# Kernel tuning notes

Measured on AMD Instinct MI355X. Metric: run time of the kernel, lower is better.

Reference implementation:

```python
import jax, jax.numpy as jnp
import numpy as np

N, D = 4096, 1024
DH = D // 2  # head=2 (forced by the two-way chunk unpack in the source)
W_SCALE = 0.02


def setup_inputs() -> dict:
    key = jax.random.key(0)
    ks = jax.random.split(key, 7)
    mk = lambda k: jax.random.normal(k, (DH, DH), dtype=jnp.float32) * W_SCALE
    return {
        "x": jax.random.normal(ks[0], (N, D), dtype=jnp.float32),
        "Wq1": mk(ks[1]), "Wq2": mk(ks[2]),
        "Wk1": mk(ks[3]), "Wk2": mk(ks[4]),
        "Wv1": mk(ks[5]), "Wv2": mk(ks[6]),
    }


def _head(xh, Wq, Wk, Wv):
    # xh: (Dh, N) channel-major chunk, W*: (Dh, Dh) 1x1-conv weights
    q = Wq @ xh  # (Dh, N)
    k = Wk @ xh  # (Dh, N)
    v = Wv @ xh  # (Dh, N)
    # QK_T conv: Sc[i, j] = k_i . q_j ; permuted -> S[j, i] = q_j . k_i
    S = jnp.einsum("dn,dm->nm", q, k)  # (N, N), no softmax / no 1/sqrt(Dh) in source
    # Sc_V conv with S as weight: out[j, d] = sum_i S[j, i] * v[d, i]
    return jnp.einsum("nm,dm->nd", S, v)  # (N, Dh)


def reference(x, Wq1, Wq2, Wk1, Wk2, Wv1, Wv2):
    xT = x.T  # (D, N), matches x.permute(1,0).reshape(D, N, 1)
    x1, x2 = xT[:DH], xT[DH:]
    o1 = _head(x1, Wq1, Wk1, Wv1)
    o2 = _head(x2, Wq2, Wk2, Wv2)
    return jnp.concatenate([o1, o2], axis=1)  # (N, D), matches concat+squeeze
```

## Files before the change

### kernel.cpp

```cpp
#include <hip/hip_runtime.h>
#include <hip/hip_bf16.h>

#define N_ROWS 4096
#define D_FULL 1024
#define DHALF  512
#define GSPLIT 8

typedef __attribute__((ext_vector_type(8))) short bf16x8;
typedef __attribute__((ext_vector_type(8))) unsigned short u16x8;
typedef __attribute__((ext_vector_type(4))) float f32x4;

__device__ __forceinline__ unsigned short f2b(float f) {
  __hip_bfloat16 h = __float2bfloat16(f);
  union { __hip_bfloat16 b; unsigned short u; } cv;
  cv.b = h;
  return cv.u;
}
__device__ __forceinline__ float b2f(unsigned short u) {
  union { unsigned int i; float f; } cv;
  cv.i = ((unsigned int)u) << 16;
  return cv.f;
}

__device__ __forceinline__ void load_lds16(const void* g, void* l) {
  __builtin_amdgcn_global_load_lds(
      (const __attribute__((address_space(1))) unsigned int*)g,
      (__attribute__((address_space(3))) unsigned int*)l, 16, 0, 0);
}

template<int N> __device__ __forceinline__ void vmwait() {
  if constexpr (N == 0)       asm volatile("s_waitcnt vmcnt(0)" ::: "memory");
  else if constexpr (N == 2)  asm volatile("s_waitcnt vmcnt(2)" ::: "memory");
  else if constexpr (N == 3)  asm volatile("s_waitcnt vmcnt(3)" ::: "memory");
  else if constexpr (N == 4)  asm volatile("s_waitcnt vmcnt(4)" ::: "memory");
  else if constexpr (N == 6)  asm volatile("s_waitcnt vmcnt(6)" ::: "memory");
  else if constexpr (N == 8)  asm volatile("s_waitcnt vmcnt(8)" ::: "memory");
  else                        asm volatile("s_waitcnt vmcnt(16)" ::: "memory");
}
__device__ __forceinline__ void barx() {
  __builtin_amdgcn_sched_barrier(0);
  __builtin_amdgcn_s_barrier();
  __builtin_amdgcn_sched_barrier(0);
}
__device__ __forceinline__ int b4inc(int b) { return (b + 1) & 3; }

__device__ __forceinline__ void cvt_tile(const float* __restrict__ src, int lds_,
                                         unsigned short* __restrict__ dst, int ldd,
                                         unsigned short* __restrict__ dstT, int ldt,
                                         int n0, int c0) {
  __shared__ unsigned short tile[64][66];
  const int t  = threadIdx.x;
  const int r  = t >> 2;
  const int cq = (t & 3) * 16;

  unsigned short loc[16];
  #pragma unroll
  for (int i = 0; i < 4; ++i) {
    float4 v = *reinterpret_cast<const float4*>(&src[(size_t)(n0 + r) * lds_ + c0 + cq + i * 4]);
    loc[i*4+0] = f2b(v.x); loc[i*4+1] = f2b(v.y); loc[i*4+2] = f2b(v.z); loc[i*4+3] = f2b(v.w);
  }
  if (dst) {
    u16x8 a, b;
    #pragma unroll
    for (int i = 0; i < 8; ++i) { a[i] = loc[i]; b[i] = loc[8+i]; }
    unsigned short* p = &dst[(size_t)(n0 + r) * ldd + c0 + cq];
    *reinterpret_cast<u16x8*>(p)     = a;
    *reinterpret_cast<u16x8*>(p + 8) = b;
  }
  if (dstT) {
    #pragma unroll
    for (int i = 0; i < 8; ++i) {
      ushort2 w2; w2.x = loc[2*i]; w2.y = loc[2*i+1];
      *reinterpret_cast<ushort2*>(&tile[r][cq + 2*i]) = w2;
    }
    __syncthreads();
    const int c  = t >> 2;
    const int ng = (t & 3) * 16;
    unsigned short o[16];
    #pragma unroll
    for (int i = 0; i < 16; ++i) o[i] = tile[ng + i][c];
    u16x8 a, b;
    #pragma unroll
    for (int i = 0; i < 8; ++i) { a[i] = o[i]; b[i] = o[8+i]; }
    unsigned short* p = &dstT[(size_t)(c0 + c) * ldt + n0 + ng];
    *reinterpret_cast<u16x8*>(p)     = a;
    *reinterpret_cast<u16x8*>(p + 8) = b;
  }
}

__global__ __launch_bounds__(256) void k_cvt_all(const float* __restrict__ x,
                                                 const float* __restrict__ w0, const float* __restrict__ w1,
                                                 const float* __restrict__ w2, const float* __restrict__ w3,
                                                 const float* __restrict__ w4, const float* __restrict__ w5,
                                                 unsigned short* __restrict__ xb,
                                                 unsigned short* __restrict__ xT,
                                                 unsigned short* __restrict__ Wb,
                                                 unsigned short* __restrict__ WbT) {
  const int b = blockIdx.x;
  if (b < 1024) {
    cvt_tile(x, D_FULL, xb, D_FULL, xT, N_ROWS, (b >> 4) * 64, (b & 15) * 64);
  } else {
    const int b2 = b - 1024;
    const int z = b2 >> 6, t = b2 & 63;
    const float* w;
    switch (z) {
      case 0: w = w0; break; case 1: w = w1; break; case 2: w = w2; break;
      case 3: w = w3; break; case 4: w = w4; break; default: w = w5; break;
    }
    const size_t HH = (size_t)DHALF * DHALF;
    unsigned short* d  = (z >= 4) ? (Wb  + z * HH) : nullptr;
    unsigned short* dT = (z <  4) ? (WbT + z * HH) : nullptr;
    cvt_tile(w, DHALF, d, DHALF, dT, DHALF, (t >> 3) * 64, (t & 7) * 64);
  }
}

__global__ __launch_bounds__(256) void k_gp(const unsigned short* __restrict__ xT,
                                            const unsigned short* __restrict__ WbT,
                                            unsigned short* __restrict__ Gp,
                                            unsigned short* __restrict__ P) {
  const int o = blockIdx.x;
  const int c = o & 7, j = o >> 3;

  const unsigned short* Ab;
  const unsigned short* Bb;
  unsigned short* Cb;
  int lda, m0, n0;
  bool sameAB = false;
  const long long HH = 262144;
  if (j < 4) {
    const int pp = c * 4 + j;
    const int h = pp >> 4, tile = pp & 15;
    Ab = WbT + (size_t)h * HH;
    Bb = WbT + (size_t)(2 + h) * HH;
    Cb = P + (size_t)h * HH;
    lda = DHALF;
    m0 = (tile >> 2) * 128; n0 = (tile & 3) * 128;
  } else {
    const int g = c * 20 + (j - 4);
    const int slice = g / 10, p = g - slice * 10;
    const int h = slice >> 3, s = slice & 7;
    const int ti = (p < 4) ? 0 : (p < 7) ? 1 : (p < 9) ? 2 : 3;
    const int tj = (p < 4) ? p : (p < 7) ? p - 3 : (p < 9) ? p - 5 : 3;
    Ab = xT + (size_t)h * DHALF * N_ROWS + s * (N_ROWS / GSPLIT);
    Bb = Ab;
    Cb = Gp + (size_t)slice * HH;
    lda = N_ROWS;
    m0 = ti * 128; n0 = tj * 128;
    sameAB = (ti == tj);
  }

  __shared__ __align__(16) unsigned short lds[4][2][128 * 32];

  const int tid  = threadIdx.x;
  const int lane = tid & 63;
  const int wave = tid >> 6;
  const int wm = (wave >> 1) * 64;
  const int wn = (wave & 1) * 64;
  const int fr = lane & 15;
  const int kg = (lane >> 4) * 8;

  const int srow = wave * 32 + (lane >> 2);
  const int scol = (lane & 3) * 8;
  const unsigned short* gA0 = Ab + (size_t)(m0 + srow) * lda + scol;
  const unsigned short* gA1 = gA0 + (size_t)16 * lda;
  const unsigned short* gB0 = Bb + (size_t)(n0 + srow) * lda + scol;
  const unsigned short* gB1 = gB0 + (size_t)16 * lda;
  const int stOff = wave * 1024;

  f32x4 acc[4][4] = {};

  auto STAGE = [&](int buf, int t) {
    const int kofs = t * 32;
    load_lds16(gA0 + kofs, &lds[buf][0][stOff]);
    load_lds16(gA1 + kofs, &lds[buf][0][stOff + 512]);
    if (!sameAB) {
      load_lds16(gB0 + kofs, &lds[buf][1][stOff]);
      load_lds16(gB1 + kofs, &lds[buf][1][stOff + 512]);
    }
  };
  auto COMPUTE = [&](int buf) {
    const unsigned short* la = &lds[buf][0][0];
    const unsigned short* lb = sameAB ? la : &lds[buf][1][0];
    bf16x8 af[4], bf[4];
    #pragma unroll
    for (int f = 0; f < 4; ++f) {
      af[f] = *reinterpret_cast<const bf16x8*>(&la[(wm + f * 16 + fr) * 32 + kg]);
      bf[f] = *reinterpret_cast<const bf16x8*>(&lb[(wn + f * 16 + fr) * 32 + kg]);
    }
    #pragma unroll
    for (int fm = 0; fm < 4; ++fm)
      #pragma unroll
      for (int fn = 0; fn < 4; ++fn)
        acc[fm][fn] = __builtin_amdgcn_mfma_f32_16x16x32_bf16(af[fm], bf[fn], acc[fm][fn], 0, 0, 0);
  };

  STAGE(0, 0); STAGE(1, 1);
  int bufS = 2, bufC = 0;
  if (sameAB) {
    for (int t = 0; t < 14; ++t) {
      STAGE(bufS, t + 2); bufS = b4inc(bufS);
      vmwait<4>(); barx();
      COMPUTE(bufC); bufC = b4inc(bufC);
    }
    vmwait<2>(); barx();
    COMPUTE(bufC); bufC = b4inc(bufC);
    vmwait<0>(); barx();
    COMPUTE(bufC);
  } else {
    for (int t = 0; t < 14; ++t) {
      STAGE(bufS, t + 2); bufS = b4inc(bufS);
      vmwait<8>(); barx();
      COMPUTE(bufC); bufC = b4inc(bufC);
    }
    vmwait<4>(); barx();
    COMPUTE(bufC); bufC = b4inc(bufC);
    vmwait<0>(); barx();
    COMPUTE(bufC);
  }

  #pragma unroll
  for (int fm = 0; fm < 4; ++fm)
    #pragma unroll
    for (int fn = 0; fn < 4; ++fn)
      #pragma unroll
      for (int r = 0; r < 4; ++r) {
        int row = m0 + wm + fm * 16 + (lane >> 4) * 4 + r;
        int col = n0 + wn + fn * 16 + fr;
        Cb[(size_t)row * DHALF + col] = f2b(acc[fm][fn][r]);
      }
}

__global__ __launch_bounds__(256) void k_gred(const unsigned short* __restrict__ Gp,
                                              unsigned short* __restrict__ G) {
  __shared__ unsigned short T[32][66];
  const int b   = blockIdx.x;
  const int h   = b >> 7;
  const int sub = b & 127;
  const int sr  = sub >> 4, sc = sub & 15;
  const int ti  = sr >> 1,  tj = sc >> 2;
  const int t   = threadIdx.x;
  const size_t HH = 262144;
  const unsigned short* gpBase = Gp + (size_t)h * GSPLIT * HH;
  unsigned short* g = G + (size_t)h * HH;

  if (ti <= tj) {
    const int r  = t >> 2;
    const int cq = (t & 3) * 8;
    const size_t off = (size_t)(sr * 64 + r) * DHALF + sc * 32 + cq;
    float sum[8] = {};
    for (int s = 0; s < GSPLIT; ++s) {
      u16x8 v = *reinterpret_cast<const u16x8*>(gpBase + (size_t)s * HH + off);
      #pragma unroll
      for (int i = 0; i < 8; ++i) sum[i] += b2f(v[i]);
    }
    u16x8 o;
    #pragma unroll
    for (int i = 0; i < 8; ++i) o[i] = f2b(sum[i]);
    *reinterpret_cast<u16x8*>(g + off) = o;
  } else {
    const int a  = t >> 3;
    const int aq = (t & 7) * 8;
    const size_t soff = (size_t)(sc * 32 + a) * DHALF + sr * 64 + aq;
    float sum[8] = {};
    for (int s = 0; s < GSPLIT; ++s) {
      u16x8 v = *reinterpret_cast<const u16x8*>(gpBase + (size_t)s * HH + soff);
      #pragma unroll
      for (int i = 0; i < 8; ++i) sum[i] += b2f(v[i]);
    }
    #pragma unroll
    for (int i = 0; i < 8; ++i) T[a][aq + i] = f2b(sum[i]);
    __syncthreads();
    const int r  = t >> 2;
    const int cq = (t & 3) * 8;
    u16x8 o;
    #pragma unroll
    for (int i = 0; i < 8; ++i) o[i] = T[cq + i][r];
    *reinterpret_cast<u16x8*>(g + (size_t)(sr * 64 + r) * DHALF + sc * 32 + cq) = o;
  }
}

__global__ __launch_bounds__(256) void k_s(const unsigned short* __restrict__ A,
                                           const unsigned short* __restrict__ B,
                                           unsigned short* __restrict__ C,
                                           long long hA, long long hB, long long hC) {
  const int o   = blockIdx.x + blockIdx.y * 8 + blockIdx.z * 64;
  const int swz = (o & 7) * 16 + (o >> 3);
  const int bx = swz & 7, by = (swz >> 3) & 7, bz = swz >> 6;

  const unsigned short* Ab = A + (size_t)bz * hA;
  const unsigned short* Bb = B + (size_t)bz * hB;
  unsigned short* Cb = C + (size_t)bz * hC;
  const int n0 = bx * 64;
  const int m0 = by * 64;

  __shared__ __align__(16) unsigned short lds[4][2][4][64 * 32];

  const int tid  = threadIdx.x;
  const int lane = tid & 63;
  const int wave = tid >> 6;
  const int wm = (wave >> 1) * 32;
  const int wn = (wave & 1) * 32;
  const int fr = lane & 15;
  const int kg = (lane >> 4) * 8;

  const int srow = lane >> 2;
  const int scol = (lane & 3) * 8;
  const unsigned short* gA = Ab + (size_t)(m0 + srow) * DHALF + wave * 32 + scol;
  const unsigned short* gB = Bb + (size_t)(n0 + srow) * DHALF + wave * 32 + scol;

  f32x4 acc[2][2] = {};

  auto STAGE = [&](int buf, int t) {
    const int kofs = t * 128;
    #pragma unroll
    for (int j = 0; j < 4; ++j) {
      load_lds16(gA + kofs + j * 16 * DHALF, &lds[buf][0][wave][j * 512]);
      load_lds16(gB + kofs + j * 16 * DHALF, &lds[buf][1][wave][j * 512]);
    }
  };
  auto COMPUTE = [&](int buf) {
    #pragma unroll
    for (int p = 0; p < 4; ++p) {
      bf16x8 a0 = *reinterpret_cast<const bf16x8*>(&lds[buf][0][p][(wm + fr) * 32 + kg]);
      bf16x8 a1 = *reinterpret_cast<const bf16x8*>(&lds[buf][0][p][(wm + 16 + fr) * 32 + kg]);
      bf16x8 b0 = *reinterpret_cast<const bf16x8*>(&lds[buf][1][p][(wn + fr) * 32 + kg]);
      bf16x8 b1 = *reinterpret_cast<const bf16x8*>(&lds[buf][1][p][(wn + 16 + fr) * 32 + kg]);
      acc[0][0] = __builtin_amdgcn_mfma_f32_16x16x32_bf16(a0, b0, acc[0][0], 0, 0, 0);
      acc[0][1] = __builtin_amdgcn_mfma_f32_16x16x32_bf16(a0, b1, acc[0][1], 0, 0, 0);
      acc[1][0] = __builtin_amdgcn_mfma_f32_16x16x32_bf16(a1, b0, acc[1][0], 0, 0, 0);
      acc[1][1] = __builtin_amdgcn_mfma_f32_16x16x32_bf16(a1, b1, acc[1][1], 0, 0, 0);
    }
  };

  STAGE(0, 0); STAGE(1, 1);
  int bufS = 2, bufC = 0;
  for (int t = 0; t < 2; ++t) {
    STAGE(bufS, t + 2); bufS = b4inc(bufS);
    vmwait<16>(); barx();
    COMPUTE(bufC); bufC = b4inc(bufC);
  }
  vmwait<8>(); barx();
  COMPUTE(bufC); bufC = b4inc(bufC);
  vmwait<0>(); barx();
  COMPUTE(bufC);

  #pragma unroll
  for (int fm = 0; fm < 2; ++fm)
    #pragma unroll
    for (int fn = 0; fn < 2; ++fn)
      #pragma unroll
      for (int r = 0; r < 4; ++r) {
        int row = m0 + wm + fm * 16 + (lane >> 4) * 4 + r;
        int col = n0 + wn + fn * 16 + fr;
        Cb[(size_t)row * DHALF + col] = f2b(acc[fm][fn][r]);
      }
}

__global__ __launch_bounds__(256) void k_final(const unsigned short* __restrict__ xb,
                                               const unsigned short* __restrict__ MT,
                                               float* __restrict__ out) {
  const int o   = blockIdx.x + blockIdx.y * 8 + blockIdx.z * 256;
  const int swz = (o & 7) * 64 + (o >> 3);
  const int bx = swz & 7, by = (swz >> 3) & 31, bz = swz >> 8;

  const unsigned short* MTh = MT + (size_t)bz * 262144;
  const int hoff = bz * DHALF;
  const int n0 = bx * 64;
  const int m0 = by * 128;

  __shared__ __align__(16) unsigned short SH[4][6144];

  const int tid  = threadIdx.x;
  const int lane = tid & 63;
  const int wave = tid >> 6;
  const int wm = (wave >> 1) * 64;
  const int wn = (wave & 1) * 32;
  const int fr = lane & 15;
  const int kg = (lane >> 4) * 8;

  const int srow = wave * 32 + (lane >> 2);
  const int scol = (lane & 3) * 8;
  const unsigned short* gA0 = xb + (size_t)(m0 + srow) * D_FULL + hoff + scol;
  const unsigned short* gA1 = gA0 + (size_t)16 * D_FULL;
  const int brow = wave * 16 + (lane >> 2);
  const unsigned short* gB = MTh + (size_t)(n0 + brow) * DHALF + scol;

  f32x4 acc[4][2] = {};

  auto STAGE = [&](int buf, int t) {
    const int kofs = t * 32;
    unsigned short* Abuf = &SH[buf][0];
    unsigned short* Bbuf = &SH[buf][4096];
    load_lds16(gA0 + kofs, Abuf + wave * 1024);
    load_lds16(gA1 + kofs, Abuf + wave * 1024 + 512);
    load_lds16(gB + kofs, Bbuf + wave * 512);
  };
  auto COMPUTE = [&](int buf) {
    unsigned short* Abuf = &SH[buf][0];
    unsigned short* Bbuf = &SH[buf][4096];
    bf16x8 af[4], bv[2];
    #pragma unroll
    for (int f = 0; f < 4; ++f)
      af[f] = *reinterpret_cast<const bf16x8*>(&Abuf[(wm + f * 16 + fr) * 32 + kg]);
    #pragma unroll
    for (int f = 0; f < 2; ++f)
      bv[f] = *reinterpret_cast<const bf16x8*>(&Bbuf[(wn + f * 16 + fr) * 32 + kg]);
    #pragma unroll
    for (int fm = 0; fm < 4; ++fm)
      #pragma unroll
      for (int fn = 0; fn < 2; ++fn)
        acc[fm][fn] = __builtin_amdgcn_mfma_f32_16x16x32_bf16(af[fm], bv[fn], acc[fm][fn], 0, 0, 0);
  };

  STAGE(0, 0); STAGE(1, 1);
  int bufS = 2, bufC = 0;
  for (int t = 0; t < 14; ++t) {
    STAGE(bufS, t + 2); bufS = b4inc(bufS);
    vmwait<6>(); barx();
    COMPUTE(bufC); bufC = b4inc(bufC);
  }
  vmwait<3>(); barx();
  COMPUTE(bufC); bufC = b4inc(bufC);
  vmwait<0>(); barx();
  COMPUTE(bufC);

  #pragma unroll
  for (int fm = 0; fm < 4; ++fm)
    #pragma unroll
    for (int fn = 0; fn < 2; ++fn)
      #pragma unroll
      for (int r = 0; r < 4; ++r) {
        int row = m0 + wm + fm * 16 + (lane >> 4) * 4 + r;
        int col = hoff + n0 + wn + fn * 16 + fr;
        out[(size_t)row * D_FULL + col] = acc[fm][fn][r];
      }
}

extern "C" void kernel_launch(void* const* d_in, const int* in_sizes, int n_in,
                              void* d_out, int out_size, void* d_ws, size_t ws_size,
                              hipStream_t stream) {
  const float* x   = (const float*)d_in[0];
  const float* Wq1 = (const float*)d_in[1];
  const float* Wq2 = (const float*)d_in[2];
  const float* Wk1 = (const float*)d_in[3];
  const float* Wk2 = (const float*)d_in[4];
  const float* Wv1 = (const float*)d_in[5];
  const float* Wv2 = (const float*)d_in[6];
  float* out = (float*)d_out;

  unsigned short* ws  = (unsigned short*)d_ws;
  unsigned short* xb  = ws;
  unsigned short* xT  = ws + 4194304;
  unsigned short* Wb  = ws + 8388608;
  unsigned short* WbT = ws + 9961472;
  unsigned short* G   = ws + 11534336;
  unsigned short* P   = ws + 12058624;
  unsigned short* TT  = ws + 12582912;
  unsigned short* MT  = ws + 13107200;
  unsigned short* Gp  = ws + 13631488;

  const long long HH = 262144;

  k_cvt_all<<<1408, 256, 0, stream>>>(x, Wq1, Wq2, Wk1, Wk2, Wv1, Wv2, xb, xT, Wb, WbT);

  k_gp<<<192, 256, 0, stream>>>(xT, WbT, Gp, P);

  k_gred<<<256, 256, 0, stream>>>(Gp, G);

  k_s<<<dim3(8, 8, 2), 256, 0, stream>>>(Wb + 4 * HH, G, TT, HH, HH, HH);
  k_s<<<dim3(8, 8, 2), 256, 0, stream>>>(TT, P, MT, HH, HH, HH);

  k_final<<<dim3(8, 32, 2), 256, 0, stream>>>(xb, MT, out);
}
```

Baseline: 44.01 us.

## Fuse split-K Gram reduction into the Wv·G GEMM kernel

Drops the separate k_gred launch. The first k_s GEMM is replaced by k_tt, which reduces the GSPLIT partial Gram matrices straight into a 64x520 shared-memory B panel, mirroring the symmetric half through a transpose tile, and then runs an MFMA GEMM against the staged Wv tiles. This removes one kernel launch and the write and re-read of G through global memory. In exchange, each block redundantly re-reduces its Gram column panel, the grid is only 128 blocks with smaller 32x32 per-wave tiles, and the reduction phase is serialized ahead of compute.

```diff
diff --git a/kernel.cpp b/kernel.cpp
--- a/kernel.cpp
+++ b/kernel.cpp
@@ -230,53 +230,133 @@
       }
 }
 
-__global__ __launch_bounds__(256) void k_gred(const unsigned short* __restrict__ Gp,
-                                              unsigned short* __restrict__ G) {
+__global__ __launch_bounds__(256) void k_tt(const unsigned short* __restrict__ Wv,
+                                            const unsigned short* __restrict__ Gp,
+                                            unsigned short* __restrict__ TT) {
+  const int o   = blockIdx.x;
+  const int swz = (o & 7) * 16 + (o >> 3);
+  const int bx = swz & 7, by = (swz >> 3) & 7, bz = swz >> 6;
+
+  const unsigned short* Ab = Wv + (size_t)bz * 262144;
+  unsigned short* Cb = TT + (size_t)bz * 262144;
+  const int n0 = bx * 64;
+  const int m0 = by * 64;
+  const int tn = bx >> 1;
+  const size_t HH = 262144;
+  const unsigned short* gpBase = Gp + (size_t)bz * GSPLIT * HH;
+
+  __shared__ __align__(16) unsigned short Bp[64 * 520];
+  __shared__ __align__(16) unsigned short lds[4][4][64 * 32];
   __shared__ unsigned short T[32][66];
-  const int b   = blockIdx.x;
-  const int h   = b >> 7;
-  const int sub = b & 127;
-  const int sr  = sub >> 4, sc = sub & 15;
-  const int ti  = sr >> 1,  tj = sc >> 2;
-  const int t   = threadIdx.x;
-  const size_t HH = 262144;
-  const unsigned short* gpBase = Gp + (size_t)h * GSPLIT * HH;
-  unsigned short* g = G + (size_t)h * HH;
-
-  if (ti <= tj) {
-    const int r  = t >> 2;
-    const int cq = (t & 3) * 8;
-    const size_t off = (size_t)(sr * 64 + r) * DHALF + sc * 32 + cq;
-    float sum[8] = {};
-    for (int s = 0; s < GSPLIT; ++s) {
-      u16x8 v = *reinterpret_cast<const u16x8*>(gpBase + (size_t)s * HH + off);
-      #pragma unroll
-      for (int i = 0; i < 8; ++i) sum[i] += b2f(v[i]);
-    }
-    u16x8 o;
-    #pragma unroll
-    for (int i = 0; i < 8; ++i) o[i] = f2b(sum[i]);
-    *reinterpret_cast<u16x8*>(g + off) = o;
-  } else {
-    const int a  = t >> 3;
-    const int aq = (t & 7) * 8;
-    const size_t soff = (size_t)(sc * 32 + a) * DHALF + sr * 64 + aq;
-    float sum[8] = {};
-    for (int s = 0; s < GSPLIT; ++s) {
-      u16x8 v = *reinterpret_cast<const u16x8*>(gpBase + (size_t)s * HH + soff);
-      #pragma unroll
-      for (int i = 0; i < 8; ++i) sum[i] += b2f(v[i]);
-    }
-    #pragma unroll
-    for (int i = 0; i < 8; ++i) T[a][aq + i] = f2b(sum[i]);
-    __syncthreads();
-    const int r  = t >> 2;
-    const int cq = (t & 3) * 8;
-    u16x8 o;
-    #pragma unroll
-    for (int i = 0; i < 8; ++i) o[i] = T[cq + i][r];
-    *reinterpret_cast<u16x8*>(g + (size_t)(sr * 64 + r) * DHALF + sc * 32 + cq) = o;
-  }
+
+  const int tid  = threadIdx.x;
+  const int lane = tid & 63;
+  const int wave = tid >> 6;
+  const int wm = (wave >> 1) * 32;
+  const int wn = (wave & 1) * 32;
+  const int fr = lane & 15;
+  const int kg = (lane >> 4) * 8;
+
+  const int srow = lane >> 2;
+  const int scol = (lane & 3) * 8;
+  const unsigned short* gA = Ab + (size_t)(m0 + srow) * DHALF + wave * 32 + scol;
+
+  auto STAGE = [&](int buf, int t) {
+    const int kofs = t * 128;
+    #pragma unroll
+    for (int j = 0; j < 4; ++j)
+      load_lds16(gA + kofs + j * 16 * DHALF, &lds[buf][wave][j * 512]);
+  };
+
+  STAGE(0, 0); STAGE(1, 1);
+
+  for (int kc = 0; kc < 4; ++kc) {
+    if (tn <= kc) {
+      const int r  = tid >> 2;
+      const int c0 = (tid & 3) * 32;
+      float s0[32];
+      #pragma unroll
+      for (int i = 0; i < 32; ++i) s0[i] = 0.f;
+      for (int s = 0; s < GSPLIT; ++s) {
+        const unsigned short* p = gpBase + (size_t)s * HH + (size_t)(n0 + r) * DHALF + kc * 128 + c0;
+        #pragma unroll
+        for (int jq = 0; jq < 4; ++jq) {
+          u16x8 v = *reinterpret_cast<const u16x8*>(p + jq * 8);
+          #pragma unroll
+          for (int i = 0; i < 8; ++i) s0[jq * 8 + i] += b2f(v[i]);
+        }
+      }
+      #pragma unroll
+      for (int jq = 0; jq < 4; ++jq) {
+        u16x8 o8;
+        #pragma unroll
+        for (int i = 0; i < 8; ++i) o8[i] = f2b(s0[jq * 8 + i]);
+        *reinterpret_cast<u16x8*>(&Bp[r * 520 + kc * 128 + c0 + jq * 8]) = o8;
+      }
+    } else {
+      for (int sp = 0; sp < 4; ++sp) {
+        const int rr = sp * 32 + (tid >> 3);
+        const int cc = (tid & 7) * 8;
+        float s0[8] = {};
+        for (int s = 0; s < GSPLIT; ++s) {
+          u16x8 v = *reinterpret_cast<const u16x8*>(
+              gpBase + (size_t)s * HH + (size_t)(kc * 128 + rr) * DHALF + n0 + cc);
+          #pragma unroll
+          for (int i = 0; i < 8; ++i) s0[i] += b2f(v[i]);
+        }
+        #pragma unroll
+        for (int i = 0; i < 8; ++i) T[tid >> 3][cc + i] = f2b(s0[i]);
+        __syncthreads();
+        const int nn = tid >> 2;
+        const int k8 = (tid & 3) * 8;
+        u16x8 o8;
+        #pragma unroll
+        for (int i = 0; i < 8; ++i) o8[i] = T[k8 + i][nn];
+        *reinterpret_cast<u16x8*>(&Bp[nn * 520 + kc * 128 + sp * 32 + k8]) = o8;
+        __syncthreads();
+      }
+    }
+  }
+  __syncthreads();
+
+  f32x4 acc[2][2] = {};
+
+  auto COMPUTE = [&](int buf, int tk) {
+    #pragma unroll
+    for (int p = 0; p < 4; ++p) {
+      const int kb = tk * 128 + p * 32;
+      bf16x8 a0 = *reinterpret_cast<const bf16x8*>(&lds[buf][p][(wm + fr) * 32 + kg]);
+      bf16x8 a1 = *reinterpret_cast<const bf16x8*>(&lds[buf][p][(wm + 16 + fr) * 32 + kg]);
+      bf16x8 b0 = *reinterpret_cast<const bf16x8*>(&Bp[(wn + fr) * 520 + kb + kg]);
+      bf16x8 b1 = *reinterpret_cast<const bf16x8*>(&Bp[(wn + 16 + fr) * 520 + kb + kg]);
+      acc[0][0] = __builtin_amdgcn_mfma_f32_16x16x32_bf16(a0, b0, acc[0][0], 0, 0, 0);
+      acc[0][1] = __builtin_amdgcn_mfma_f32_16x16x32_bf16(a0, b1, acc[0][1], 0, 0, 0);
+      acc[1][0] = __builtin_amdgcn_mfma_f32_16x16x32_bf16(a1, b0, acc[1][0], 0, 0, 0);
+      acc[1][1] = __builtin_amdgcn_mfma_f32_16x16x32_bf16(a1, b1, acc[1][1], 0, 0, 0);
+    }
+  };
+
+  int bufS = 2, bufC = 0;
+  for (int t = 0; t < 2; ++t) {
+    STAGE(bufS, t + 2); bufS = b4inc(bufS);
+    vmwait<8>(); barx();
+    COMPUTE(bufC, t); bufC = b4inc(bufC);
+  }
+  vmwait<4>(); barx();
+  COMPUTE(bufC, 2); bufC = b4inc(bufC);
+  vmwait<0>(); barx();
+  COMPUTE(bufC, 3);
+
+  #pragma unroll
+  for (int fm = 0; fm < 2; ++fm)
+    #pragma unroll
+    for (int fn = 0; fn < 2; ++fn)
+      #pragma unroll
+      for (int r = 0; r < 4; ++r) {
+        int row = m0 + wm + fm * 16 + (lane >> 4) * 4 + r;
+        int col = n0 + wn + fn * 16 + fr;
+        Cb[(size_t)row * DHALF + col] = f2b(acc[fm][fn][r]);
+      }
 }
 
 __global__ __launch_bounds__(256) void k_s(const unsigned short* __restrict__ A,
@@ -453,7 +533,6 @@
   unsigned short* xT  = ws + 4194304;
   unsigned short* Wb  = ws + 8388608;
   unsigned short* WbT = ws + 9961472;
-  unsigned short* G   = ws + 11534336;
   unsigned short* P   = ws + 12058624;
   unsigned short* TT  = ws + 12582912;
   unsigned short* MT  = ws + 13107200;
@@ -465,9 +544,8 @@
 
   k_gp<<<192, 256, 0, stream>>>(xT, WbT, Gp, P);
 
-  k_gred<<<256, 256, 0, stream>>>(Gp, G);
-
-  k_s<<<dim3(8, 8, 2), 256, 0, stream>>>(Wb + 4 * HH, G, TT, HH, HH, HH);
+  k_tt<<<128, 256, 0, stream>>>(Wb + 4 * HH, Gp, TT);
+
   k_s<<<dim3(8, 8, 2), 256, 0, stream>>>(TT, P, MT, HH, HH, HH);
 
   k_final<<<dim3(8, 32, 2), 256, 0, stream>>>(xb, MT, out);
```

Result: slower. 52.95 us (+20.3%).
